# Kernel tuning notes

Measured on AMD Instinct MI355X. Metric: run time of the kernel, lower is better.

Reference implementation:

```python
import jax, jax.numpy as jnp
import numpy as np

B, NQ, NK, C = 8, 1024, 1024, 1024
H, DK, DV = 16, 64, 64


def setup_inputs() -> dict:
    key = jax.random.key(0)
    ks = jax.random.split(key, 10)
    queries = jax.random.normal(ks[0], (B, NQ, C), dtype=jnp.float32)
    keys_ = jax.random.normal(ks[1], (B, NK, C), dtype=jnp.float32)
    values = jax.random.normal(ks[2], (B, NK, C), dtype=jnp.float32)
    attention_mask = jax.random.randint(ks[3], (B, H, NQ, NK), 0, 2).astype(jnp.bool_)
    attention_weights = jax.random.uniform(ks[4], (B, H, NQ, NK), dtype=jnp.float32)
    std = 0.001  # init.normal_(m.weight, std=0.001), bias=0
    Wq = jax.random.normal(ks[5], (C, H * DK), dtype=jnp.float32) * std
    Wk = jax.random.normal(ks[6], (C, H * DK), dtype=jnp.float32) * std
    Wv = jax.random.normal(ks[7], (C, H * DV), dtype=jnp.float32) * std
    Wo = jax.random.normal(ks[8], (H * DV, C), dtype=jnp.float32) * std
    bq = jnp.zeros((H * DK,), jnp.float32)
    bk = jnp.zeros((H * DK,), jnp.float32)
    bv = jnp.zeros((H * DV,), jnp.float32)
    bo = jnp.zeros((C,), jnp.float32)
    return {"queries": queries, "keys": keys_, "values": values,
            "attention_mask": attention_mask, "attention_weights": attention_weights,
            "Wq": Wq, "bq": bq, "Wk": Wk, "bk": bk, "Wv": Wv, "bv": bv,
            "Wo": Wo, "bo": bo}


def reference(queries, keys, values, attention_mask, attention_weights,
              Wq, bq, Wk, bk, Wv, bv, Wo, bo):
    bs, nq, _ = queries.shape
    nk = keys.shape[1]
    # projections -> (b, h, n, d)
    q = (queries @ Wq + bq).reshape(bs, nq, H, DK).transpose(0, 2, 1, 3)
    k = (keys @ Wk + bk).reshape(bs, nk, H, DK).transpose(0, 2, 1, 3)
    v = (values @ Wv + bv).reshape(bs, nk, H, DV).transpose(0, 2, 1, 3)
    att = jnp.einsum('bhqd,bhkd->bhqk', q, k) / np.sqrt(DK).astype(np.float32)
    att = att * attention_weights
    att = jnp.where(attention_mask, -jnp.inf, att)
    att = jax.nn.softmax(att, axis=-1)
    # dropout is identity in eval mode
    out = jnp.einsum('bhqk,bhkd->bhqd', att, v)
    out = out.transpose(0, 2, 1, 3).reshape(bs, nq, H * DV)
    return out @ Wo + bo
```

## Files before the change

### kernel.cpp

```cpp
#include <hip/hip_runtime.h>
#include <hip/hip_bf16.h>

using short8 = __attribute__((ext_vector_type(8))) short;
using f32x4  = __attribute__((ext_vector_type(4))) float;

__device__ __forceinline__ unsigned short f2bf(float f) {
    union { float f; unsigned u; } x; x.f = f;
    unsigned r = x.u + 0x7FFFu + ((x.u >> 16) & 1u);
    return (unsigned short)(r >> 16);
}

__device__ __forceinline__ void gload_lds16(const void* g, void* l) {
    __builtin_amdgcn_global_load_lds(
        (const __attribute__((address_space(1))) unsigned int*)g,
        (__attribute__((address_space(3))) unsigned int*)l, 16, 0, 0);
}

__global__ void detect_mask_kernel(const unsigned int* __restrict__ m, int* __restrict__ flag) {
    if (threadIdx.x == 0) *flag = 0;
    __syncthreads();
    unsigned v = m[threadIdx.x];
    if (v > 1u) {
        atomicOr(flag, 1);
        if (v != 0x3F800000u) atomicOr(flag, 2);
    }
}

__global__ __launch_bounds__(256) void maskpack_kernel(
    const void* __restrict__ mask, const int* __restrict__ flag,
    unsigned long long* __restrict__ Mb, int nwords)
{
    const int l = threadIdx.x & 63;
    const int gwave = (int)((blockIdx.x * 256 + threadIdx.x) >> 6);
    const int nw = (int)((gridDim.x * 256) >> 6);
    const bool bytem = ((*flag) & 2) != 0;
    const unsigned char* m8 = (const unsigned char*)mask;
    const unsigned int* m32 = (const unsigned int*)mask;
    for (int w0 = gwave * 4; w0 < nwords; w0 += nw * 4) {
        unsigned v[4];
#pragma unroll
        for (int u = 0; u < 4; u++) {
            size_t e = (size_t)(w0 + u) * 64 + l;
            v[u] = bytem ? (unsigned)m8[e] : m32[e];
        }
#pragma unroll
        for (int u = 0; u < 4; u++) {
            unsigned long long b = __ballot(v[u] != 0u);
            if (l == 0) Mb[w0 + u] = b;
        }
    }
}

__global__ __launch_bounds__(256) void wconv_kernel(
    const float* __restrict__ W0, const float* __restrict__ W1,
    const float* __restrict__ W2, const float* __restrict__ W3,
    unsigned short* __restrict__ Wt)
{
    const int z = blockIdx.z;
    const float* W = (z == 0) ? W0 : ((z == 1) ? W1 : ((z == 2) ? W2 : W3));
    unsigned short* O = Wt + (size_t)z * 1024 * 1024;
    __shared__ float tile[64][68];
    const int t = threadIdx.x;
    const int k0 = blockIdx.x * 64, n0 = blockIdx.y * 64;
    const int rr = t >> 4, cc = t & 15;
#pragma unroll
    for (int i = 0; i < 4; i++) {
        int row = rr + i * 16;
        float4 v = *reinterpret_cast<const float4*>(W + (size_t)(k0 + row) * 1024 + n0 + cc * 4);
        *reinterpret_cast<float4*>(&tile[row][cc * 4]) = v;
    }
    __syncthreads();
#pragma unroll
    for (int i = 0; i < 4; i++) {
        int rn = rr + i * 16;
        ushort4 ov;
        ov.x = f2bf(tile[cc * 4 + 0][rn]);
        ov.y = f2bf(tile[cc * 4 + 1][rn]);
        ov.z = f2bf(tile[cc * 4 + 2][rn]);
        ov.w = f2bf(tile[cc * 4 + 3][rn]);
        *reinterpret_cast<ushort4*>(O + (size_t)(n0 + rn) * 1024 + k0 + cc * 4) = ov;
    }
}

__global__ __launch_bounds__(256) void aconv_kernel(
    const float* __restrict__ Aq, const float* __restrict__ Ak, const float* __restrict__ Av,
    unsigned short* __restrict__ Out)
{
    const int z = blockIdx.y;
    const float* A = (z == 0) ? Aq : ((z == 1) ? Ak : Av);
    unsigned short* O = Out + (size_t)z * 8192 * 1024;
    size_t i = ((size_t)blockIdx.x * 256 + threadIdx.x) * 8;
    float4 v0 = *reinterpret_cast<const float4*>(A + i);
    float4 v1 = *reinterpret_cast<const float4*>(A + i + 4);
    short8 o;
    o[0] = (short)f2bf(v0.x); o[1] = (short)f2bf(v0.y);
    o[2] = (short)f2bf(v0.z); o[3] = (short)f2bf(v0.w);
    o[4] = (short)f2bf(v1.x); o[5] = (short)f2bf(v1.y);
    o[6] = (short)f2bf(v1.z); o[7] = (short)f2bf(v1.w);
    *reinterpret_cast<short8*>(O + i) = o;
}

#define GEMM_IT(KT, RB, SB, DOST, WN)                                                       \
    {                                                                                       \
        if (DOST) {                                                                         \
            const int ko = ((KT) + 2) * 64;                                                 \
            gload_lds16(gA0 + ko, lA0_##SB); gload_lds16(gA1 + ko, lA1_##SB);               \
            gload_lds16(gB0 + ko, lB0_##SB); gload_lds16(gB1 + ko, lB1_##SB);               \
        }                                                                                   \
        short8 af[4], bfm[4];                                                               \
        _Pragma("unroll")                                                                   \
        for (int fr = 0; fr < 4; fr++)                                                      \
            af[fr] = *reinterpret_cast<const short8*>(rdA + (RB) * 8192 + fr * 1024);       \
        _Pragma("unroll")                                                                   \
        for (int fc = 0; fc < 4; fc++)                                                      \
            bfm[fc] = *reinterpret_cast<const short8*>(rdB + (RB) * 8192 + fc * 1024);      \
        _Pragma("unroll")                                                                   \
        for (int fr = 0; fr < 4; fr++)                                                      \
            _Pragma("unroll")                                                               \
            for (int fc = 0; fc < 4; fc++)                                                  \
                acc[fr][fc] = __builtin_amdgcn_mfma_f32_16x16x32_bf16(af[fr], bfm[fc], acc[fr][fc], 0, 0, 0); \
        asm volatile("s_waitcnt vmcnt(" #WN ")" ::: "memory");                              \
        __builtin_amdgcn_s_barrier();                                                       \
        __builtin_amdgcn_sched_barrier(0);                                                  \
    }

#define GEMM_IT_LAST(RB)                                                                    \
    {                                                                                       \
        short8 af[4], bfm[4];                                                               \
        _Pragma("unroll")                                                                   \
        for (int fr = 0; fr < 4; fr++)                                                      \
            af[fr] = *reinterpret_cast<const short8*>(rdA + (RB) * 8192 + fr * 1024);       \
        _Pragma("unroll")                                                                   \
        for (int fc = 0; fc < 4; fc++)                                                      \
            bfm[fc] = *reinterpret_cast<const short8*>(rdB + (RB) * 8192 + fc * 1024);      \
        _Pragma("unroll")                                                                   \
        for (int fr = 0; fr < 4; fr++)                                                      \
            _Pragma("unroll")                                                               \
            for (int fc = 0; fc < 4; fc++)                                                  \
                acc[fr][fc] = __builtin_amdgcn_mfma_f32_16x16x32_bf16(af[fr], bfm[fc], acc[fr][fc], 0, 0, 0); \
    }

#define GEMM_CORE(A_PTR, W_PTR)                                                             \
    __shared__ unsigned short Ab[3][4096];                                                  \
    __shared__ unsigned short Bb[3][4096];                                                  \
    const int tid = threadIdx.x, w = tid >> 6, l = tid & 63, l16 = l & 15, g = l >> 4;      \
    const int wr = w >> 1, wc = w & 1;                                                      \
    const int row0 = blockIdx.x * 128, col0 = blockIdx.y * 128;                             \
    const int offs = tid * 16;                                                              \
    const char* gA0 = (const char*)(A_PTR) + (size_t)(row0 + (offs >> 6)) * 2048 + (offs & 63);          \
    const char* gA1 = (const char*)(A_PTR) + (size_t)(row0 + ((offs + 4096) >> 6)) * 2048 + (offs & 63); \
    const char* gB0 = (const char*)(W_PTR) + (size_t)(col0 + (offs >> 6)) * 2048 + (offs & 63);          \
    const char* gB1 = (const char*)(W_PTR) + (size_t)(col0 + ((offs + 4096) >> 6)) * 2048 + (offs & 63); \
    char* lA0_0 = (char*)Ab[0] + w * 1024; char* lA1_0 = (char*)Ab[0] + 4096 + w * 1024;    \
    char* lA0_1 = (char*)Ab[1] + w * 1024; char* lA1_1 = (char*)Ab[1] + 4096 + w * 1024;    \
    char* lA0_2 = (char*)Ab[2] + w * 1024; char* lA1_2 = (char*)Ab[2] + 4096 + w * 1024;    \
    char* lB0_0 = (char*)Bb[0] + w * 1024; char* lB1_0 = (char*)Bb[0] + 4096 + w * 1024;    \
    char* lB0_1 = (char*)Bb[1] + w * 1024; char* lB1_1 = (char*)Bb[1] + 4096 + w * 1024;    \
    char* lB0_2 = (char*)Bb[2] + w * 1024; char* lB1_2 = (char*)Bb[2] + 4096 + w * 1024;    \
    const char* rdA = (char*)Ab[0] + (wr * 64 + l16) * 64 + g * 16;                         \
    const char* rdB = (char*)Bb[0] + (wc * 64 + l16) * 64 + g * 16;                         \
    f32x4 acc[4][4];                                                                        \
    _Pragma("unroll")                                                                       \
    for (int i = 0; i < 4; i++)                                                             \
        _Pragma("unroll")                                                                   \
        for (int j = 0; j < 4; j++) acc[i][j] = (f32x4){0.f, 0.f, 0.f, 0.f};                \
    gload_lds16(gA0, lA0_0); gload_lds16(gA1, lA1_0);                                       \
    gload_lds16(gB0, lB0_0); gload_lds16(gB1, lB1_0);                                       \
    gload_lds16(gA0 + 64, lA0_1); gload_lds16(gA1 + 64, lA1_1);                             \
    gload_lds16(gB0 + 64, lB0_1); gload_lds16(gB1 + 64, lB1_1);                             \
    asm volatile("s_waitcnt vmcnt(4)" ::: "memory");                                        \
    __builtin_amdgcn_s_barrier();                                                           \
    __builtin_amdgcn_sched_barrier(0);                                                      \
    for (int kt0 = 0; kt0 < 30; kt0 += 3) {                                                 \
        GEMM_IT(kt0 + 0, 0, 2, 1, 4)                                                        \
        GEMM_IT(kt0 + 1, 1, 0, 1, 4)                                                        \
        GEMM_IT(kt0 + 2, 2, 1, 1, 4)                                                        \
    }                                                                                       \
    GEMM_IT(30, 0, 0, 0, 0)                                                                 \
    GEMM_IT_LAST(1)

__global__ __launch_bounds__(256, 3) void gemm_proj_kernel(
    const unsigned short* __restrict__ Abf,
    const unsigned short* __restrict__ Wt,
    const float* __restrict__ bq, const float* __restrict__ bk, const float* __restrict__ bv,
    unsigned short* __restrict__ Out)
{
    const int z = blockIdx.z;
    const unsigned short* A = Abf + (size_t)z * 8192 * 1024;
    const unsigned short* Wz = Wt + (size_t)z * 1024 * 1024;
    const float* bias = (z == 0) ? bq : ((z == 1) ? bk : bv);
    unsigned short* Oz = Out + (size_t)z * 8 * 16 * 1024 * 64;

    GEMM_CORE(A, Wz)

#pragma unroll
    for (int fr = 0; fr < 4; fr++)
#pragma unroll
        for (int fc = 0; fc < 4; fc++)
#pragma unroll
            for (int r = 0; r < 4; r++) {
                int row = row0 + wr * 64 + fr * 16 + g * 4 + r;
                int col = col0 + wc * 64 + fc * 16 + l16;
                float val = acc[fr][fc][r] + bias[col];
                int bb = row >> 10, n = row & 1023;
                int h = col >> 6, d = col & 63;
                Oz[(((size_t)(bb * 16 + h)) * 1024 + n) * 64 + d] = f2bf(val);
            }
}

__global__ __launch_bounds__(256, 3) void gemm_out_kernel(
    const unsigned short* __restrict__ Ain,
    const unsigned short* __restrict__ Wto,
    const float* __restrict__ bo,
    float* __restrict__ Out)
{
    GEMM_CORE(Ain, Wto)

#pragma unroll
    for (int fr = 0; fr < 4; fr++)
#pragma unroll
        for (int fc = 0; fc < 4; fc++)
#pragma unroll
            for (int r = 0; r < 4; r++) {
                int row = row0 + wr * 64 + fr * 16 + g * 4 + r;
                int col = col0 + wc * 64 + fc * 16 + l16;
                Out[(size_t)row * 1024 + col] = acc[fr][fc][r] + bo[col];
            }
}

__global__ __launch_bounds__(256) void proj_f32_kernel(
    const float* __restrict__ Aq, const float* __restrict__ Ak, const float* __restrict__ Av,
    const unsigned short* __restrict__ Wt,
    const float* __restrict__ bq, const float* __restrict__ bk, const float* __restrict__ bv,
    unsigned short* __restrict__ Out)
{
    const int z = blockIdx.z;
    const float* A = (z == 0) ? Aq : ((z == 1) ? Ak : Av);
    const float* bias = (z == 0) ? bq : ((z == 1) ? bk : bv);
    const unsigned short* Wz = Wt + (size_t)z * 1024 * 1024;
    unsigned short* Oz = Out + (size_t)z * 8 * 16 * 1024 * 64;

    const int tid = threadIdx.x;
    const int w = tid >> 6, l = tid & 63;
    const int l16 = l & 15, g = l >> 4;
    const int rbase = blockIdx.x * 128 + w * 32;
    const int cbase = blockIdx.y * 64;

    f32x4 acc[2][4];
#pragma unroll
    for (int i = 0; i < 2; i++)
#pragma unroll
        for (int j = 0; j < 4; j++) acc[i][j] = (f32x4){0.f, 0.f, 0.f, 0.f};

#pragma unroll 2
    for (int k0 = 0; k0 < 1024; k0 += 32) {
        short8 a[2];
#pragma unroll
        for (int rf = 0; rf < 2; rf++) {
            const float* ap = A + (size_t)(rbase + rf * 16 + l16) * 1024 + k0 + g * 8;
            float4 v0 = *reinterpret_cast<const float4*>(ap);
            float4 v1 = *reinterpret_cast<const float4*>(ap + 4);
            short8 av;
            av[0] = (short)f2bf(v0.x); av[1] = (short)f2bf(v0.y);
            av[2] = (short)f2bf(v0.z); av[3] = (short)f2bf(v0.w);
            av[4] = (short)f2bf(v1.x); av[5] = (short)f2bf(v1.y);
            av[6] = (short)f2bf(v1.z); av[7] = (short)f2bf(v1.w);
            a[rf] = av;
        }
        short8 bfr[4];
#pragma unroll
        for (int cf = 0; cf < 4; cf++)
            bfr[cf] = *reinterpret_cast<const short8*>(Wz + (size_t)(cbase + cf * 16 + l16) * 1024 + k0 + g * 8);
#pragma unroll
        for (int rf = 0; rf < 2; rf++)
#pragma unroll
            for (int cf = 0; cf < 4; cf++)
                acc[rf][cf] = __builtin_amdgcn_mfma_f32_16x16x32_bf16(a[rf], bfr[cf], acc[rf][cf], 0, 0, 0);
    }

#pragma unroll
    for (int rf = 0; rf < 2; rf++)
#pragma unroll
        for (int cf = 0; cf < 4; cf++)
#pragma unroll
            for (int r = 0; r < 4; r++) {
                int row = rbase + rf * 16 + g * 4 + r;
                int col = cbase + cf * 16 + l16;
                float val = acc[rf][cf][r] + bias[col];
                int bb = row >> 10, n = row & 1023;
                int h = col >> 6, d = col & 63;
                Oz[(((size_t)(bb * 16 + h)) * 1024 + n) * 64 + d] = f2bf(val);
            }
}

__global__ __launch_bounds__(256) void vtrans_kernel(
    const unsigned short* __restrict__ Vs, unsigned short* __restrict__ Vt)
{
    const int bh = blockIdx.y;
    const int k0 = blockIdx.x * 64;
    const unsigned short* In = Vs + (size_t)bh * 1024 * 64;
    unsigned short* O = Vt + (size_t)bh * 64 * 1024;
    __shared__ unsigned short tile[64][72];
    const int t = threadIdx.x;
    {
        const int row = t >> 3;
        const int c8 = (t & 7) * 8;
#pragma unroll
        for (int i = 0; i < 2; i++) {
            int r = row + i * 32;
            short8 v = *reinterpret_cast<const short8*>(In + (size_t)(k0 + r) * 64 + c8);
            *reinterpret_cast<short8*>(&tile[r][c8]) = v;
        }
    }
    __syncthreads();
    {
        const int rd = t >> 4, c4 = (t & 15) * 4;
#pragma unroll
        for (int i = 0; i < 4; i++) {
            int d = rd + i * 16;
            ushort4 ov;
            ov.x = tile[c4 + 0][d];
            ov.y = tile[c4 + 1][d];
            ov.z = tile[c4 + 2][d];
            ov.w = tile[c4 + 3][d];
            *reinterpret_cast<ushort4*>(O + (size_t)d * 1024 + k0 + c4) = ov;
        }
    }
}

__global__ __launch_bounds__(512, 1) void attn_kernel(
    const unsigned short* __restrict__ Qs,
    const unsigned short* __restrict__ Ks,
    const unsigned short* __restrict__ Vt,
    const float* __restrict__ attw,
    const unsigned long long* __restrict__ Mb,
    unsigned short* __restrict__ AO)
{
    extern __shared__ char smem[];

    const int bid = blockIdx.x;
    const int xj = bid & 7, xp = bid >> 3;
    const int qt = xp & 7;
    const int gbh = (xp >> 3) * 8 + xj;
    const int h = gbh & 15, b = gbh >> 4;
    const int bh = b * 16 + h;

    const int tid = threadIdx.x, w = tid >> 6, l = tid & 63, l16 = l & 15, g = l >> 4;
    const int myq = qt * 128 + w * 16 + l16;

    const unsigned short* Qbh = Qs + (size_t)bh * 65536;
    const char* Kb = (const char*)(Ks + (size_t)bh * 65536);
    const char* Vb = (const char*)(Vt + (size_t)bh * 65536);
    const float* wrow = attw + ((size_t)bh * 1024 + myq) * 1024;
    const unsigned long long* mrow = Mb + ((size_t)bh * 1024 + myq) * 16;

    const int kb_swz = ((l & 7) * 16) ^ ((l >> 3) << 4);
    const char* gKb = Kb + (size_t)(w * 16 + (l >> 3)) * 128 + kb_swz;
    const int vrow0 = w * 8 + (l >> 4);
    const char* gVb0 = Vb + (size_t)vrow0 * 2048 + (((l & 15) * 16) ^ ((vrow0 & 7) << 4));
    const char* gVb1 = Vb + (size_t)(vrow0 + 4) * 2048 + (((l & 15) * 16) ^ (((vrow0 + 4) & 7) << 4));

    const int swz = (l16 & 7) << 4;
    const int krdA = l16 * 128 + ((g * 16) ^ swz);
    const int krdB = l16 * 128 + ((64 + g * 16) ^ swz);
    char* const pbase = smem + 65536 + w * 4096 + l16 * 256;

    gload_lds16(gKb, smem + w * 2048);
    gload_lds16(gKb + 1024, smem + w * 2048 + 1024);
    gload_lds16(gVb0, smem + 32768 + w * 2048);
    gload_lds16(gVb1, smem + 32768 + w * 2048 + 1024);
    __builtin_amdgcn_sched_barrier(0);

    short8 qf0 = *reinterpret_cast<const short8*>(Qbh + (size_t)myq * 64 + g * 8);
    short8 qf1 = *reinterpret_cast<const short8*>(Qbh + (size_t)myq * 64 + 32 + g * 8);
    float4 wv[8];
    unsigned long long mb0, mb1;
#pragma unroll
    for (int cf = 0; cf < 8; cf++)
        wv[cf] = *reinterpret_cast<const float4*>(wrow + cf * 16 + g * 4);
    mb0 = mrow[0];
    mb1 = mrow[1];

    asm volatile("s_waitcnt vmcnt(12)" ::: "memory");
    __builtin_amdgcn_s_barrier();
    __builtin_amdgcn_sched_barrier(0);

    f32x4 accO[4];
#pragma unroll
    for (int j = 0; j < 4; j++) accO[j] = (f32x4){0.f, 0.f, 0.f, 0.f};
    float den = 0.f;

#define ATTN_BODY(CURK)                                                                     \
    _Pragma("unroll")                                                                       \
    for (int cf = 0; cf < 8; cf++) {                                                        \
        short8 k0 = *reinterpret_cast<const short8*>(smem + (CURK) + krdA + cf * 2048);     \
        short8 k1 = *reinterpret_cast<const short8*>(smem + (CURK) + krdB + cf * 2048);     \
        f32x4 s = (f32x4){0.f, 0.f, 0.f, 0.f};                                              \
        s = __builtin_amdgcn_mfma_f32_16x16x32_bf16(k0, qf0, s, 0, 0, 0);                   \
        s = __builtin_amdgcn_mfma_f32_16x16x32_bf16(k1, qf1, s, 0, 0, 0);                   \
        unsigned mn = (unsigned)((cf < 4 ? mb0 >> (cf * 16 + g * 4)                         \
                                         : mb1 >> ((cf - 4) * 16 + g * 4))) & 0xFu;         \
        float p0 = (mn & 1u) ? 0.f : __expf(s[0] * 0.125f * wv[cf].x);                      \
        float p1 = (mn & 2u) ? 0.f : __expf(s[1] * 0.125f * wv[cf].y);                      \
        float p2 = (mn & 4u) ? 0.f : __expf(s[2] * 0.125f * wv[cf].z);                      \
        float p3 = (mn & 8u) ? 0.f : __expf(s[3] * 0.125f * wv[cf].w);                      \
        den += p0 + p1 + p2 + p3;                                                           \
        ushort4 pwv;                                                                        \
        pwv.x = f2bf(p0); pwv.y = f2bf(p1); pwv.z = f2bf(p2); pwv.w = f2bf(p3);             \
        *reinterpret_cast<ushort4*>(pbase + ((cf * 32 + g * 8) ^ swz)) = pwv;               \
    }

#define ATTN_PV(CURV)                                                                       \
    _Pragma("unroll")                                                                       \
    for (int ks = 0; ks < 4; ks++) {                                                        \
        short8 pf = *reinterpret_cast<const short8*>(pbase + ((ks * 64 + g * 16) ^ swz));   \
        _Pragma("unroll")                                                                   \
        for (int cd = 0; cd < 4; cd++) {                                                    \
            short8 vf = *reinterpret_cast<const short8*>(                                   \
                smem + 32768 + (CURV) + (cd * 16 + l16) * 256 + ((ks * 64 + g * 16) ^ swz));\
            accO[cd] = __builtin_amdgcn_mfma_f32_16x16x32_bf16(pf, vf, accO[cd], 0, 0, 0);  \
        }                                                                                   \
    }

    for (int t = 0; t < 7; t++) {
        const int cur = (t & 1) * 16384, nxt = 16384 - cur;
        gload_lds16(gKb + (size_t)(t + 1) * 16384, smem + nxt + w * 2048);
        gload_lds16(gKb + (size_t)(t + 1) * 16384 + 1024, smem + nxt + w * 2048 + 1024);
        gload_lds16(gVb0 + (size_t)(t + 1) * 256, smem + 32768 + nxt + w * 2048);
        gload_lds16(gVb1 + (size_t)(t + 1) * 256, smem + 32768 + nxt + w * 2048 + 1024);
        __builtin_amdgcn_sched_barrier(0);

        ATTN_BODY(cur)

#pragma unroll
        for (int cf = 0; cf < 8; cf++)
            wv[cf] = *reinterpret_cast<const float4*>(wrow + (t + 1) * 128 + cf * 16 + g * 4);
        mb0 = mrow[2 * (t + 1)];
        mb1 = mrow[2 * (t + 1) + 1];

        ATTN_PV(cur)

        asm volatile("s_waitcnt vmcnt(10)" ::: "memory");
        __builtin_amdgcn_s_barrier();
        __builtin_amdgcn_sched_barrier(0);
    }
    ATTN_BODY(16384)
    ATTN_PV(16384)
#undef ATTN_BODY
#undef ATTN_PV

    den += __shfl_xor(den, 16);
    den += __shfl_xor(den, 32);

#pragma unroll
    for (int r = 0; r < 4; r++) {
        float dr = __shfl(den, g * 4 + r);
        float inv = 1.0f / dr;
#pragma unroll
        for (int cd = 0; cd < 4; cd++) {
            int qrow = qt * 128 + w * 16 + g * 4 + r;
            int col = h * 64 + cd * 16 + l16;
            AO[((size_t)b * 1024 + qrow) * 1024 + col] = f2bf(accO[cd][r] * inv);
        }
    }
}

extern "C" void kernel_launch(void* const* d_in, const int* in_sizes, int n_in,
                              void* d_out, int out_size, void* d_ws, size_t ws_size,
                              hipStream_t stream)
{
    const float* queries = (const float*)d_in[0];
    const float* keys    = (const float*)d_in[1];
    const float* values  = (const float*)d_in[2];
    const void*  mask    = d_in[3];
    const float* attw    = (const float*)d_in[4];
    const float* Wq = (const float*)d_in[5];
    const float* bq = (const float*)d_in[6];
    const float* Wk = (const float*)d_in[7];
    const float* bk = (const float*)d_in[8];
    const float* Wv = (const float*)d_in[9];
    const float* bv = (const float*)d_in[10];
    const float* Wo = (const float*)d_in[11];
    const float* bo = (const float*)d_in[12];

    char* ws = (char*)d_ws;
    int* flag = (int*)ws;
    unsigned short* base = (unsigned short*)(ws + 256);
    const size_t M8 = (size_t)8 * 1024 * 1024;
    unsigned short* Qs  = base;
    unsigned short* Ksb = base + M8;
    unsigned short* Vs  = base + 2 * M8;
    unsigned short* Vtb = base + 3 * M8;
    unsigned short* AO  = base + 4 * M8;
    unsigned short* Wt  = base + 5 * M8;
    unsigned short* Abf = base + 5 * M8 + 4 * 1024 * 1024;
    unsigned long long* Mb = (unsigned long long*)Vs;
    const size_t need_abf = 256 + (5 * M8 + 4 * 1024 * 1024 + 3 * M8) * sizeof(unsigned short);
    const bool useAbf = ws_size >= need_abf;

    detect_mask_kernel<<<1, 256, 0, stream>>>((const unsigned int*)mask, flag);
    wconv_kernel<<<dim3(16, 16, 4), 256, 0, stream>>>(Wq, Wk, Wv, Wo, Wt);
    if (useAbf) {
        aconv_kernel<<<dim3(4096, 3), 256, 0, stream>>>(queries, keys, values, Abf);
        gemm_proj_kernel<<<dim3(64, 8, 3), 256, 0, stream>>>(Abf, Wt, bq, bk, bv, Qs);
    } else {
        proj_f32_kernel<<<dim3(64, 16, 3), 256, 0, stream>>>(queries, keys, values, Wt, bq, bk, bv, Qs);
    }
    vtrans_kernel<<<dim3(16, 128), 256, 0, stream>>>(Vs, Vtb);
    maskpack_kernel<<<dim3(2048), 256, 0, stream>>>(mask, flag, Mb, 2 * 1024 * 1024);
    attn_kernel<<<dim3(1024), 512, 98304, stream>>>(Qs, Ksb, Vtb, attw, Mb, AO);
    gemm_out_kernel<<<dim3(64, 8), 256, 0, stream>>>(AO, Wt + (size_t)3 * 1024 * 1024, bo, (float*)d_out);
}
```

Baseline: 413.8 us.

## Replace projection GEMM with 256x256-tile, 8-wave, double-buffered LDS kernel

The QKV projection GEMM moves from a 128x128 tile with 4 waves (3-stage LDS ring) to a 256x256 tile with 8 waves, using 128 KB of dynamic LDS that double-buffers 128-wide K slices through swizzled global_load_lds. Each wave now computes a 128x64 output sub-tile with 32 accumulators, interleaving prefetch of the next K slice with MFMA and raising wave priority during the MFMA blocks. The aim is higher arithmetic intensity and less global/LDS traffic per FLOP. In exchange it needs more registers, allows only one block per CU because of the large LDS footprint, and launches fewer blocks (384), which may leave some CUs idle at the tail.

```diff
diff --git a/kernel.cpp b/kernel.cpp
--- a/kernel.cpp
+++ b/kernel.cpp
@@ -98,6 +98,105 @@
     o[4] = (short)f2bf(v1.x); o[5] = (short)f2bf(v1.y);
     o[6] = (short)f2bf(v1.z); o[7] = (short)f2bf(v1.w);
     *reinterpret_cast<short8*>(O + i) = o;
+}
+
+__global__ __launch_bounds__(512, 2) void gemm_proj8_kernel(
+    const unsigned short* __restrict__ Abf,
+    const unsigned short* __restrict__ Wt,
+    const float* __restrict__ bq, const float* __restrict__ bk, const float* __restrict__ bv,
+    unsigned short* __restrict__ Out)
+{
+    extern __shared__ char smem[];
+    const int z = blockIdx.z;
+    const unsigned short* A = Abf + (size_t)z * 8192 * 1024;
+    const unsigned short* Wz = Wt + (size_t)z * 1024 * 1024;
+    const float* bias = (z == 0) ? bq : ((z == 1) ? bk : bv);
+    unsigned short* Oz = Out + (size_t)z * 8 * 16 * 1024 * 64;
+
+    const int tid = threadIdx.x, w = tid >> 6, l = tid & 63, l16 = l & 15, g = l >> 4;
+    const int wm = w >> 2, wn = w & 3;
+    const int row0 = blockIdx.x * 256, col0 = blockIdx.y * 256;
+
+    const int csrc = ((l & 7) * 16) ^ ((l >> 5) << 5);
+    const char* gA = (const char*)A + (size_t)(row0 + w * 16 + (l >> 3)) * 2048 + csrc;
+    const char* gB = (const char*)Wz + (size_t)(col0 + w * 16 + (l >> 3)) * 2048 + csrc;
+
+    const int sw = ((l16 >> 2) & 1) << 5;
+    const int ard = (wm * 128 + l16) * 128 + ((g * 16) ^ sw);
+    const int brd = (wn * 64 + l16) * 128 + ((g * 16) ^ sw);
+
+    f32x4 acc[8][4];
+#pragma unroll
+    for (int i = 0; i < 8; i++)
+#pragma unroll
+        for (int j = 0; j < 4; j++) acc[i][j] = (f32x4){0.f, 0.f, 0.f, 0.f};
+
+#pragma unroll
+    for (int h = 0; h < 2; h++) {
+        gload_lds16(gA + h * 262144, smem + h * 16384 + w * 2048);
+        gload_lds16(gA + h * 262144 + 16384, smem + h * 16384 + w * 2048 + 1024);
+        gload_lds16(gB + h * 262144, smem + 65536 + h * 16384 + w * 2048);
+        gload_lds16(gB + h * 262144 + 16384, smem + 65536 + h * 16384 + w * 2048 + 1024);
+    }
+    asm volatile("s_waitcnt vmcnt(0)" ::: "memory");
+    __builtin_amdgcn_s_barrier();
+    __builtin_amdgcn_sched_barrier(0);
+
+    for (int t = 0; t < 16; t++) {
+        const int buf = (t & 1) * 32768, nbuf = 32768 - buf;
+        const int dost = (t < 15);
+        const size_t knext = (size_t)(t + 1) * 128;
+#pragma unroll
+        for (int p = 0; p < 4; p++) {
+            const int kk = p & 1, mh = p >> 1;
+            short8 a[4], bm[4];
+#pragma unroll
+            for (int mf = 0; mf < 4; mf++)
+                a[mf] = *reinterpret_cast<const short8*>(
+                    smem + buf + ard + mh * 8192 + mf * 2048 + kk * 64);
+#pragma unroll
+            for (int nf = 0; nf < 4; nf++)
+                bm[nf] = *reinterpret_cast<const short8*>(
+                    smem + 65536 + buf + brd + nf * 2048 + kk * 64);
+            if (dost) {
+                if (p < 2) {
+                    gload_lds16(gA + p * 262144 + knext, smem + nbuf + p * 16384 + w * 2048);
+                    gload_lds16(gA + p * 262144 + 16384 + knext, smem + nbuf + p * 16384 + w * 2048 + 1024);
+                } else {
+                    gload_lds16(gB + (p - 2) * 262144 + knext, smem + 65536 + nbuf + (p - 2) * 16384 + w * 2048);
+                    gload_lds16(gB + (p - 2) * 262144 + 16384 + knext, smem + 65536 + nbuf + (p - 2) * 16384 + w * 2048 + 1024);
+                }
+            }
+            __builtin_amdgcn_s_barrier();
+            asm volatile("s_waitcnt lgkmcnt(0)" ::: "memory");
+            __builtin_amdgcn_sched_barrier(0);
+            __builtin_amdgcn_s_setprio(1);
+#pragma unroll
+            for (int mf = 0; mf < 4; mf++)
+#pragma unroll
+                for (int nf = 0; nf < 4; nf++)
+                    acc[mh * 4 + mf][nf] = __builtin_amdgcn_mfma_f32_16x16x32_bf16(
+                        a[mf], bm[nf], acc[mh * 4 + mf][nf], 0, 0, 0);
+            __builtin_amdgcn_s_setprio(0);
+            if (p == 3) asm volatile("s_waitcnt vmcnt(0)" ::: "memory");
+            __builtin_amdgcn_s_barrier();
+            __builtin_amdgcn_sched_barrier(0);
+        }
+    }
+
+#pragma unroll
+    for (int mf8 = 0; mf8 < 8; mf8++)
+#pragma unroll
+        for (int nf = 0; nf < 4; nf++)
+#pragma unroll
+            for (int r = 0; r < 4; r++) {
+                int row = row0 + wm * 128 + mf8 * 16 + g * 4 + r;
+                int col = col0 + wn * 64 + nf * 16 + l16;
+                float val = acc[mf8][nf][r] + bias[col];
+                int bb = row >> 10, n = row & 1023;
+                int h = col >> 6, d = col & 63;
+                Oz[(((size_t)(bb * 16 + h)) * 1024 + n) * 64 + d] = f2bf(val);
+            }
 }
 
 #define GEMM_IT(KT, RB, SB, DOST, WN)                                                       \
@@ -179,35 +278,6 @@
     GEMM_IT(30, 0, 0, 0, 0)                                                                 \
     GEMM_IT_LAST(1)
 
-__global__ __launch_bounds__(256, 3) void gemm_proj_kernel(
-    const unsigned short* __restrict__ Abf,
-    const unsigned short* __restrict__ Wt,
-    const float* __restrict__ bq, const float* __restrict__ bk, const float* __restrict__ bv,
-    unsigned short* __restrict__ Out)
-{
-    const int z = blockIdx.z;
-    const unsigned short* A = Abf + (size_t)z * 8192 * 1024;
-    const unsigned short* Wz = Wt + (size_t)z * 1024 * 1024;
-    const float* bias = (z == 0) ? bq : ((z == 1) ? bk : bv);
-    unsigned short* Oz = Out + (size_t)z * 8 * 16 * 1024 * 64;
-
-    GEMM_CORE(A, Wz)
-
-#pragma unroll
-    for (int fr = 0; fr < 4; fr++)
-#pragma unroll
-        for (int fc = 0; fc < 4; fc++)
-#pragma unroll
-            for (int r = 0; r < 4; r++) {
-                int row = row0 + wr * 64 + fr * 16 + g * 4 + r;
-                int col = col0 + wc * 64 + fc * 16 + l16;
-                float val = acc[fr][fc][r] + bias[col];
-                int bb = row >> 10, n = row & 1023;
-                int h = col >> 6, d = col & 63;
-                Oz[(((size_t)(bb * 16 + h)) * 1024 + n) * 64 + d] = f2bf(val);
-            }
-}
-
 __global__ __launch_bounds__(256, 3) void gemm_out_kernel(
     const unsigned short* __restrict__ Ain,
     const unsigned short* __restrict__ Wto,
@@ -502,7 +572,7 @@
     wconv_kernel<<<dim3(16, 16, 4), 256, 0, stream>>>(Wq, Wk, Wv, Wo, Wt);
     if (useAbf) {
         aconv_kernel<<<dim3(4096, 3), 256, 0, stream>>>(queries, keys, values, Abf);
-        gemm_proj_kernel<<<dim3(64, 8, 3), 256, 0, stream>>>(Abf, Wt, bq, bk, bv, Qs);
+        gemm_proj8_kernel<<<dim3(32, 4, 3), 512, 131072, stream>>>(Abf, Wt, bq, bk, bv, Qs);
     } else {
         proj_f32_kernel<<<dim3(64, 16, 3), 256, 0, stream>>>(queries, keys, values, Wt, bq, bk, bv, Qs);
     }
```

New measurement: 427.5 us. +3.3%, slower.

## Rework projection GEMMs to 256x128 tiles with 8 waves and swizzled LDS

Applied to the files above, without the earlier changes.

Both bf16 GEMMs (QKV projection and output projection) move from 128x128 tiles with 4 waves to 256x128 tiles with 8 waves, using dynamic shared memory and a three-stage ring of global-to-LDS loads. The LDS layout is XOR-swizzled to cut bank conflicts. The MFMA work is split into two half-tiles with s_setprio around the math. The aim is more data reuse per block and better overlap of LDS reads with MFMA. The cost is more barriers per k-step, and the larger tiles halve the grid size, which may reduce occupancy and tail balance.

```diff
diff --git a/kernel.cpp b/kernel.cpp
--- a/kernel.cpp
+++ b/kernel.cpp
@@ -100,86 +100,80 @@
     *reinterpret_cast<short8*>(O + i) = o;
 }
 
-#define GEMM_IT(KT, RB, SB, DOST, WN)                                                       \
+#define P8_STAGE(T2, BS)                                                                    \
+    gload_lds16(gA0 + (size_t)(T2) * 64, smem + (BS) * 16384 + w * 1024);                   \
+    gload_lds16(gA1 + (size_t)(T2) * 64, smem + (BS) * 16384 + 8192 + w * 1024);            \
+    gload_lds16(gBp + (size_t)(T2) * 64, smem + 49152 + (BS) * 8192 + w * 1024);
+
+#define P8_TILE(T, BR, BS, DOST, DOW, WN)                                                   \
     {                                                                                       \
-        if (DOST) {                                                                         \
-            const int ko = ((KT) + 2) * 64;                                                 \
-            gload_lds16(gA0 + ko, lA0_##SB); gload_lds16(gA1 + ko, lA1_##SB);               \
-            gload_lds16(gB0 + ko, lB0_##SB); gload_lds16(gB1 + ko, lB1_##SB);               \
-        }                                                                                   \
-        short8 af[4], bfm[4];                                                               \
-        _Pragma("unroll")                                                                   \
-        for (int fr = 0; fr < 4; fr++)                                                      \
-            af[fr] = *reinterpret_cast<const short8*>(rdA + (RB) * 8192 + fr * 1024);       \
-        _Pragma("unroll")                                                                   \
-        for (int fc = 0; fc < 4; fc++)                                                      \
-            bfm[fc] = *reinterpret_cast<const short8*>(rdB + (RB) * 8192 + fc * 1024);      \
-        _Pragma("unroll")                                                                   \
-        for (int fr = 0; fr < 4; fr++)                                                      \
+        if (DOST) { P8_STAGE((T) + 2, BS) }                                                 \
+        short8 a0[4], bb[2], a1[4];                                                         \
+        _Pragma("unroll")                                                                   \
+        for (int mf = 0; mf < 4; mf++)                                                      \
+            a0[mf] = *reinterpret_cast<const short8*>(smem + (BR) * 16384 + ard + mf * 1024); \
+        _Pragma("unroll")                                                                   \
+        for (int nf = 0; nf < 2; nf++)                                                      \
+            bb[nf] = *reinterpret_cast<const short8*>(smem + 49152 + (BR) * 8192 + brd + nf * 1024); \
+        __builtin_amdgcn_s_barrier();                                                       \
+        asm volatile("s_waitcnt lgkmcnt(0)" ::: "memory");                                  \
+        __builtin_amdgcn_sched_barrier(0);                                                  \
+        __builtin_amdgcn_s_setprio(1);                                                      \
+        _Pragma("unroll")                                                                   \
+        for (int mf = 0; mf < 4; mf++)                                                      \
             _Pragma("unroll")                                                               \
-            for (int fc = 0; fc < 4; fc++)                                                  \
-                acc[fr][fc] = __builtin_amdgcn_mfma_f32_16x16x32_bf16(af[fr], bfm[fc], acc[fr][fc], 0, 0, 0); \
-        asm volatile("s_waitcnt vmcnt(" #WN ")" ::: "memory");                              \
+            for (int nf = 0; nf < 2; nf++)                                                  \
+                acc[mf][nf] = __builtin_amdgcn_mfma_f32_16x16x32_bf16(a0[mf], bb[nf], acc[mf][nf], 0, 0, 0); \
+        __builtin_amdgcn_s_setprio(0);                                                      \
+        _Pragma("unroll")                                                                   \
+        for (int mf = 0; mf < 4; mf++)                                                      \
+            a1[mf] = *reinterpret_cast<const short8*>(smem + (BR) * 16384 + 4096 + ard + mf * 1024); \
+        __builtin_amdgcn_s_barrier();                                                       \
+        asm volatile("s_waitcnt lgkmcnt(0)" ::: "memory");                                  \
+        __builtin_amdgcn_sched_barrier(0);                                                  \
+        __builtin_amdgcn_s_setprio(1);                                                      \
+        _Pragma("unroll")                                                                   \
+        for (int mf = 0; mf < 4; mf++)                                                      \
+            _Pragma("unroll")                                                               \
+            for (int nf = 0; nf < 2; nf++)                                                  \
+                acc[4 + mf][nf] = __builtin_amdgcn_mfma_f32_16x16x32_bf16(a1[mf], bb[nf], acc[4 + mf][nf], 0, 0, 0); \
+        __builtin_amdgcn_s_setprio(0);                                                      \
+        if (DOW) { asm volatile("s_waitcnt vmcnt(" #WN ")" ::: "memory"); }                 \
         __builtin_amdgcn_s_barrier();                                                       \
         __builtin_amdgcn_sched_barrier(0);                                                  \
     }
 
-#define GEMM_IT_LAST(RB)                                                                    \
-    {                                                                                       \
-        short8 af[4], bfm[4];                                                               \
-        _Pragma("unroll")                                                                   \
-        for (int fr = 0; fr < 4; fr++)                                                      \
-            af[fr] = *reinterpret_cast<const short8*>(rdA + (RB) * 8192 + fr * 1024);       \
-        _Pragma("unroll")                                                                   \
-        for (int fc = 0; fc < 4; fc++)                                                      \
-            bfm[fc] = *reinterpret_cast<const short8*>(rdB + (RB) * 8192 + fc * 1024);      \
-        _Pragma("unroll")                                                                   \
-        for (int fr = 0; fr < 4; fr++)                                                      \
-            _Pragma("unroll")                                                               \
-            for (int fc = 0; fc < 4; fc++)                                                  \
-                acc[fr][fc] = __builtin_amdgcn_mfma_f32_16x16x32_bf16(af[fr], bfm[fc], acc[fr][fc], 0, 0, 0); \
-    }
-
-#define GEMM_CORE(A_PTR, W_PTR)                                                             \
-    __shared__ unsigned short Ab[3][4096];                                                  \
-    __shared__ unsigned short Bb[3][4096];                                                  \
+#define GEMM8_CORE(A_PTR, W_PTR)                                                            \
+    extern __shared__ char smem[];                                                          \
     const int tid = threadIdx.x, w = tid >> 6, l = tid & 63, l16 = l & 15, g = l >> 4;      \
-    const int wr = w >> 1, wc = w & 1;                                                      \
-    const int row0 = blockIdx.x * 128, col0 = blockIdx.y * 128;                             \
-    const int offs = tid * 16;                                                              \
-    const char* gA0 = (const char*)(A_PTR) + (size_t)(row0 + (offs >> 6)) * 2048 + (offs & 63);          \
-    const char* gA1 = (const char*)(A_PTR) + (size_t)(row0 + ((offs + 4096) >> 6)) * 2048 + (offs & 63); \
-    const char* gB0 = (const char*)(W_PTR) + (size_t)(col0 + (offs >> 6)) * 2048 + (offs & 63);          \
-    const char* gB1 = (const char*)(W_PTR) + (size_t)(col0 + ((offs + 4096) >> 6)) * 2048 + (offs & 63); \
-    char* lA0_0 = (char*)Ab[0] + w * 1024; char* lA1_0 = (char*)Ab[0] + 4096 + w * 1024;    \
-    char* lA0_1 = (char*)Ab[1] + w * 1024; char* lA1_1 = (char*)Ab[1] + 4096 + w * 1024;    \
-    char* lA0_2 = (char*)Ab[2] + w * 1024; char* lA1_2 = (char*)Ab[2] + 4096 + w * 1024;    \
-    char* lB0_0 = (char*)Bb[0] + w * 1024; char* lB1_0 = (char*)Bb[0] + 4096 + w * 1024;    \
-    char* lB0_1 = (char*)Bb[1] + w * 1024; char* lB1_1 = (char*)Bb[1] + 4096 + w * 1024;    \
-    char* lB0_2 = (char*)Bb[2] + w * 1024; char* lB1_2 = (char*)Bb[2] + 4096 + w * 1024;    \
-    const char* rdA = (char*)Ab[0] + (wr * 64 + l16) * 64 + g * 16;                         \
-    const char* rdB = (char*)Bb[0] + (wc * 64 + l16) * 64 + g * 16;                         \
-    f32x4 acc[4][4];                                                                        \
+    const int wm = w >> 2, wn = w & 3;                                                      \
+    const int row0 = blockIdx.x * 256, col0 = blockIdx.y * 128;                             \
+    const int csrc = ((l & 3) * 16) ^ (((l >> 3) & 3) << 4);                                \
+    const char* gA0 = (const char*)(A_PTR) + (size_t)(row0 + w * 16 + (l >> 2)) * 2048 + csrc; \
+    const char* gA1 = gA0 + (size_t)128 * 2048;                                             \
+    const char* gBp = (const char*)(W_PTR) + (size_t)(col0 + w * 16 + (l >> 2)) * 2048 + csrc; \
+    const int sw = ((l16 >> 1) & 3) << 4;                                                   \
+    const int ard = (wm * 128 + l16) * 64 + ((g * 16) ^ sw);                                \
+    const int brd = (wn * 32 + l16) * 64 + ((g * 16) ^ sw);                                 \
+    f32x4 acc[8][2];                                                                        \
     _Pragma("unroll")                                                                       \
-    for (int i = 0; i < 4; i++)                                                             \
-        _Pragma("unroll")                                                                   \
-        for (int j = 0; j < 4; j++) acc[i][j] = (f32x4){0.f, 0.f, 0.f, 0.f};                \
-    gload_lds16(gA0, lA0_0); gload_lds16(gA1, lA1_0);                                       \
-    gload_lds16(gB0, lB0_0); gload_lds16(gB1, lB1_0);                                       \
-    gload_lds16(gA0 + 64, lA0_1); gload_lds16(gA1 + 64, lA1_1);                             \
-    gload_lds16(gB0 + 64, lB0_1); gload_lds16(gB1 + 64, lB1_1);                             \
-    asm volatile("s_waitcnt vmcnt(4)" ::: "memory");                                        \
+    for (int i = 0; i < 8; i++)                                                             \
+        _Pragma("unroll")                                                                   \
+        for (int j = 0; j < 2; j++) acc[i][j] = (f32x4){0.f, 0.f, 0.f, 0.f};                \
+    P8_STAGE(0, 0)                                                                          \
+    P8_STAGE(1, 1)                                                                          \
+    asm volatile("s_waitcnt vmcnt(3)" ::: "memory");                                        \
     __builtin_amdgcn_s_barrier();                                                           \
     __builtin_amdgcn_sched_barrier(0);                                                      \
-    for (int kt0 = 0; kt0 < 30; kt0 += 3) {                                                 \
-        GEMM_IT(kt0 + 0, 0, 2, 1, 4)                                                        \
-        GEMM_IT(kt0 + 1, 1, 0, 1, 4)                                                        \
-        GEMM_IT(kt0 + 2, 2, 1, 1, 4)                                                        \
+    for (int tb = 0; tb < 30; tb += 3) {                                                    \
+        P8_TILE(tb + 0, 0, 2, 1, 1, 3)                                                      \
+        P8_TILE(tb + 1, 1, 0, 1, 1, 3)                                                      \
+        P8_TILE(tb + 2, 2, 1, 1, 1, 3)                                                      \
     }                                                                                       \
-    GEMM_IT(30, 0, 0, 0, 0)                                                                 \
-    GEMM_IT_LAST(1)
-
-__global__ __launch_bounds__(256, 3) void gemm_proj_kernel(
+    P8_TILE(30, 0, 0, 0, 1, 0)                                                              \
+    P8_TILE(31, 1, 0, 0, 0, 0)
+
+__global__ __launch_bounds__(512, 4) void gemm_proj8_kernel(
     const unsigned short* __restrict__ Abf,
     const unsigned short* __restrict__ Wt,
     const float* __restrict__ bq, const float* __restrict__ bk, const float* __restrict__ bv,
@@ -191,40 +185,40 @@
     const float* bias = (z == 0) ? bq : ((z == 1) ? bk : bv);
     unsigned short* Oz = Out + (size_t)z * 8 * 16 * 1024 * 64;
 
-    GEMM_CORE(A, Wz)
-
-#pragma unroll
-    for (int fr = 0; fr < 4; fr++)
-#pragma unroll
-        for (int fc = 0; fc < 4; fc++)
+    GEMM8_CORE(A, Wz)
+
+#pragma unroll
+    for (int mf8 = 0; mf8 < 8; mf8++)
+#pragma unroll
+        for (int nf = 0; nf < 2; nf++)
 #pragma unroll
             for (int r = 0; r < 4; r++) {
-                int row = row0 + wr * 64 + fr * 16 + g * 4 + r;
-                int col = col0 + wc * 64 + fc * 16 + l16;
-                float val = acc[fr][fc][r] + bias[col];
+                int row = row0 + wm * 128 + mf8 * 16 + g * 4 + r;
+                int col = col0 + wn * 32 + nf * 16 + l16;
+                float val = acc[mf8][nf][r] + bias[col];
                 int bb = row >> 10, n = row & 1023;
-                int h = col >> 6, d = col & 63;
-                Oz[(((size_t)(bb * 16 + h)) * 1024 + n) * 64 + d] = f2bf(val);
+                int hh = col >> 6, d = col & 63;
+                Oz[(((size_t)(bb * 16 + hh)) * 1024 + n) * 64 + d] = f2bf(val);
             }
 }
 
-__global__ __launch_bounds__(256, 3) void gemm_out_kernel(
+__global__ __launch_bounds__(512, 4) void gemm_out8_kernel(
     const unsigned short* __restrict__ Ain,
     const unsigned short* __restrict__ Wto,
     const float* __restrict__ bo,
     float* __restrict__ Out)
 {
-    GEMM_CORE(Ain, Wto)
-
-#pragma unroll
-    for (int fr = 0; fr < 4; fr++)
-#pragma unroll
-        for (int fc = 0; fc < 4; fc++)
+    GEMM8_CORE(Ain, Wto)
+
+#pragma unroll
+    for (int mf8 = 0; mf8 < 8; mf8++)
+#pragma unroll
+        for (int nf = 0; nf < 2; nf++)
 #pragma unroll
             for (int r = 0; r < 4; r++) {
-                int row = row0 + wr * 64 + fr * 16 + g * 4 + r;
-                int col = col0 + wc * 64 + fc * 16 + l16;
-                Out[(size_t)row * 1024 + col] = acc[fr][fc][r] + bo[col];
+                int row = row0 + wm * 128 + mf8 * 16 + g * 4 + r;
+                int col = col0 + wn * 32 + nf * 16 + l16;
+                Out[(size_t)row * 1024 + col] = acc[mf8][nf][r] + bo[col];
             }
 }
 
@@ -502,12 +496,12 @@
     wconv_kernel<<<dim3(16, 16, 4), 256, 0, stream>>>(Wq, Wk, Wv, Wo, Wt);
     if (useAbf) {
         aconv_kernel<<<dim3(4096, 3), 256, 0, stream>>>(queries, keys, values, Abf);
-        gemm_proj_kernel<<<dim3(64, 8, 3), 256, 0, stream>>>(Abf, Wt, bq, bk, bv, Qs);
+        gemm_proj8_kernel<<<dim3(32, 8, 3), 512, 73728, stream>>>(Abf, Wt, bq, bk, bv, Qs);
     } else {
         proj_f32_kernel<<<dim3(64, 16, 3), 256, 0, stream>>>(queries, keys, values, Wt, bq, bk, bv, Qs);
     }
     vtrans_kernel<<<dim3(16, 128), 256, 0, stream>>>(Vs, Vtb);
     maskpack_kernel<<<dim3(2048), 256, 0, stream>>>(mask, flag, Mb, 2 * 1024 * 1024);
     attn_kernel<<<dim3(1024), 512, 98304, stream>>>(Qs, Ksb, Vtb, attw, Mb, AO);
-    gemm_out_kernel<<<dim3(64, 8), 256, 0, stream>>>(AO, Wt + (size_t)3 * 1024 * 1024, bo, (float*)d_out);
-}
+    gemm_out8_kernel<<<dim3(32, 8), 512, 73728, stream>>>(AO, Wt + (size_t)3 * 1024 * 1024, bo, (float*)d_out);
+}
```

Measured after the change: 397.5 us, median of 2. 3.9% less time.
